# Performance work log

Measured on AMD Instinct MI355X. Metric: run time of the kernel, lower is better.

## Reference

```python
import jax, jax.numpy as jnp
import numpy as np

N_QUBITS = 12
N_LAYERS = 6
BATCH = 512
DIM = 2 ** N_QUBITS


def _apply_1q(psi, G, wire):
    """Apply a single-qubit gate on `wire` (wire 0 = most significant).
    psi: [B, 2^n] complex. G: [2,2] (shared) or [B,2,2] (batched)."""
    B = psi.shape[0]
    left = 2 ** wire
    psi = psi.reshape(B, left, 2, -1)
    if G.ndim == 2:
        psi = jnp.einsum('ij,bxjy->bxiy', G, psi)
    else:
        psi = jnp.einsum('bij,bxjy->bxiy', G, psi)
    return psi.reshape(B, -1)


def _apply_cnot(psi, c, t):
    """CNOT with control c, target t on [B, 2^n] state."""
    B = psi.shape[0]
    ps = psi.reshape((B,) + (2,) * N_QUBITS)
    ca, ta = c + 1, t + 1
    c0 = jnp.take(ps, 0, axis=ca)
    c1 = jnp.take(ps, 1, axis=ca)
    flip_ax = ta if ta < ca else ta - 1
    c1 = jnp.flip(c1, axis=flip_ax)  # X on target within control=1 block
    ps = jnp.stack([c0, c1], axis=ca)
    return ps.reshape(B, -1)


def _circuit(x, weights):
    B = x.shape[0]
    psi = jnp.zeros((B, DIM), jnp.complex64).at[:, 0].set(1.0)

    # AngleEmbedding: RY(x_w) on each wire (batched gate matrices)
    h = 0.5 * x
    c, s = jnp.cos(h).astype(jnp.complex64), jnp.sin(h).astype(jnp.complex64)
    for w in range(N_QUBITS):
        G = jnp.stack([jnp.stack([c[:, w], -s[:, w]], -1),
                       jnp.stack([s[:, w], c[:, w]], -1)], -2)  # [B,2,2]
        psi = _apply_1q(psi, G, w)

    # StronglyEntanglingLayers: Rot(phi,theta,omega) per wire, then ring of CNOTs
    for l in range(N_LAYERS):
        phi, theta, omega = weights[l, :, 0], weights[l, :, 1], weights[l, :, 2]
        ct = jnp.cos(0.5 * theta).astype(jnp.complex64)
        st = jnp.sin(0.5 * theta).astype(jnp.complex64)
        ep = jnp.exp(-0.5j * (phi + omega).astype(jnp.complex64))
        em = jnp.exp(0.5j * (phi - omega).astype(jnp.complex64))
        # Rot = RZ(omega) RY(theta) RZ(phi)
        m00 = ep * ct
        m01 = -em * st
        m10 = jnp.conj(em) * st
        m11 = jnp.conj(ep) * ct
        for w in range(N_QUBITS):
            G = jnp.array([[m00[w], m01[w]], [m10[w], m11[w]]], jnp.complex64)
            psi = _apply_1q(psi, G, w)
        r = l % (N_QUBITS - 1) + 1
        for w in range(N_QUBITS):
            psi = _apply_cnot(psi, w, (w + r) % N_QUBITS)

    # <Z_w> for every wire
    probs = psi.real ** 2 + psi.imag ** 2  # [B, 2^n]
    exps = []
    for w in range(N_QUBITS):
        p = probs.reshape(B, 2 ** w, 2, -1)
        exps.append(p[:, :, 0, :].sum((1, 2)) - p[:, :, 1, :].sum((1, 2)))
    return jnp.stack(exps, -1)  # [B, n_qubits]


def setup_inputs() -> dict:
    key = jax.random.key(0)
    k1, k2, k3, k4 = jax.random.split(key, 4)
    x = jax.random.uniform(k1, (BATCH, N_QUBITS), jnp.float32, -np.pi, np.pi)
    weights = jax.random.uniform(k2, (N_LAYERS, N_QUBITS, 3), jnp.float32, 0.0, 2.0 * np.pi)
    W = jax.random.normal(k3, (1, N_QUBITS), jnp.float32) * 0.3
    b = jax.random.normal(k4, (1,), jnp.float32) * 0.01
    return {"x": x, "weights": weights, "W": W, "b": b}


def reference(x, weights, W, b):
    z = _circuit(x, weights)              # [B, n_qubits]
    y = z @ W.T + b                       # [B, 1]
    return y.squeeze(-1)                  # [B]
```

## Files before the change

### kernel.cpp

```cpp
#include <hip/hip_runtime.h>
#include <stdint.h>

#define NQ 12
#define DIM 4096
#define NLAYERS 6
#define TPB 256

typedef float v2f __attribute__((ext_vector_type(2)));

struct Pass_t {
    uint32_t WT[8];
    uint32_t WL[8];
    uint32_t RT[8];
    uint32_t RL[16];
};
struct Pass10_t {
    uint32_t WT[6];
    uint32_t WL[8];
    uint32_t RT[6];
    uint32_t RL[16];
};
struct CK_t {
    Pass10_t PA;
    Pass_t PB;
    Pass_t P1[NLAYERS];
    uint32_t frow[NQ];
};

constexpr uint32_t G2f(uint32_t k){ return ((k&15u)<<8) | (k&0xF0u) | ((k>>8)&15u); }
constexpr uint32_t G3f(uint32_t k){ return ((k&15u)<<4) | ((k>>4)&15u) | (k&0xF00u); }

constexpr uint32_t ech_reduce(const uint32_t* v, int n, uint32_t x){
    bool ch = true;
    while (ch) {
        ch = false;
        for (int i = 0; i < n; i++)
            if (v[i] && (x ^ v[i]) < x) { x ^= v[i]; ch = true; }
    }
    return x;
}

constexpr Pass_t build_pass(const uint32_t* Mc) {
    Pass_t P{};
    uint32_t rows[12]{};
    rows[0] = 8u;
    int nr = 1;
    uint32_t full[12]{}; int nf = 0; full[nf++] = 8u;
    uint32_t We[4]{};  int nw = 0;
    uint32_t Re[5]{};  int nre = 0;
    {
        uint32_t p0 = 0;
        for (int j = 0; j < 5; j++)
            p0 |= (uint32_t)(__builtin_popcount(8u & Mc[4 + j]) & 1) << j;
        uint32_t r = ech_reduce(Re, nre, p0);
        if (r) Re[nre++] = r;
    }
    for (int slot = 0; slot < 4; slot++) {
        uint32_t chosen = 0;
        for (int relax = 0; relax < 3 && !chosen; relax++) {
            for (uint32_t m = 1; m < 4096u && !chosen; m++) {
                if (m & 8u) continue;
                uint32_t wp = (m >> 4) & 15u;
                uint32_t wr = ech_reduce(We, nw, wp);
                if (relax < 2 && !wr) continue;
                uint32_t rp = 0;
                for (int j = 0; j < 5; j++)
                    rp |= (uint32_t)(__builtin_popcount(m & Mc[4 + j]) & 1) << j;
                uint32_t rr = ech_reduce(Re, nre, rp);
                if (relax < 1 && !rr) continue;
                uint32_t fr = ech_reduce(full, nf, m);
                if (!fr) continue;
                chosen = m; full[nf++] = fr;
                if (wr && nw < 4) We[nw++] = wr;
                if (rr && nre < 5) Re[nre++] = rr;
            }
        }
        rows[nr++] = chosen;
    }
    for (int slot = nr; slot < 12; slot++) {
        for (uint32_t m = 1; m < 4096u; m++) {
            if (m & 8u) continue;
            uint32_t fr = ech_reduce(full, nf, m);
            if (fr) { rows[slot] = m; full[nf++] = fr; break; }
        }
    }
    uint32_t col[12]{}, lmc[12]{};
    for (int j = 0; j < 12; j++) {
        uint32_t c = 0;
        for (int i = 0; i < 12; i++) c |= (uint32_t)((rows[i] >> j) & 1u) << i;
        col[j] = c;
    }
    for (int j = 0; j < 12; j++) {
        uint32_t a = 0, mc = Mc[j];
        for (int q = 0; q < 12; q++) if ((mc >> q) & 1u) a ^= col[q];
        lmc[j] = a;
    }
    for (int j = 0; j < 8; j++) { P.WT[j] = col[4 + j]; P.RT[j] = lmc[4 + j]; }
    for (int j = 0; j < 8; j++) {
        uint32_t a = 0;
        for (int q = 0; q < 3; q++) if ((j >> q) & 1) a ^= col[q];
        P.WL[j] = a;
    }
    for (int l = 0; l < 16; l++) {
        uint32_t a = 0;
        for (int q = 0; q < 4; q++) if ((l >> q) & 1) a ^= lmc[q];
        P.RL[l] = a;
    }
    return P;
}

constexpr Pass10_t build_pass10(const uint32_t* Mc) {
    Pass10_t P{};
    uint32_t rows[10]{};
    rows[0] = 8u;
    int nr = 1;
    uint32_t full[10]{}; int nf = 0; full[nf++] = 8u;
    uint32_t We[4]{};  int nw = 0;
    uint32_t Re[5]{};  int nre = 0;
    {
        uint32_t p0 = 0;
        for (int j = 0; j < 5; j++)
            p0 |= (uint32_t)(__builtin_popcount(8u & Mc[4 + j]) & 1) << j;
        uint32_t r = ech_reduce(Re, nre, p0);
        if (r) Re[nre++] = r;
    }
    for (int slot = 0; slot < 4; slot++) {
        uint32_t chosen = 0;
        for (int relax = 0; relax < 3 && !chosen; relax++) {
            for (uint32_t m = 1; m < 1024u && !chosen; m++) {
                if (m & 8u) continue;
                uint32_t wp = (m >> 4) & 15u;
                uint32_t wr = ech_reduce(We, nw, wp);
                if (relax < 2 && !wr) continue;
                uint32_t rp = 0;
                for (int j = 0; j < 5; j++)
                    rp |= (uint32_t)(__builtin_popcount(m & Mc[4 + j]) & 1) << j;
                uint32_t rr = ech_reduce(Re, nre, rp);
                if (relax < 1 && !rr) continue;
                uint32_t fr = ech_reduce(full, nf, m);
                if (!fr) continue;
                chosen = m; full[nf++] = fr;
                if (wr && nw < 4) We[nw++] = wr;
                if (rr && nre < 5) Re[nre++] = rr;
            }
        }
        rows[nr++] = chosen;
    }
    for (int slot = nr; slot < 10; slot++) {
        for (uint32_t m = 1; m < 1024u; m++) {
            if (m & 8u) continue;
            uint32_t fr = ech_reduce(full, nf, m);
            if (fr) { rows[slot] = m; full[nf++] = fr; break; }
        }
    }
    uint32_t col[10]{}, lmc[10]{};
    for (int j = 0; j < 10; j++) {
        uint32_t c = 0;
        for (int i = 0; i < 10; i++) c |= (uint32_t)((rows[i] >> j) & 1u) << i;
        col[j] = c;
    }
    for (int j = 0; j < 10; j++) {
        uint32_t a = 0, mc = Mc[j];
        for (int q = 0; q < 10; q++) if ((mc >> q) & 1u) a ^= col[q];
        lmc[j] = a;
    }
    for (int j = 0; j < 6; j++) { P.WT[j] = col[4 + j]; P.RT[j] = lmc[4 + j]; }
    for (int j = 0; j < 8; j++) {
        uint32_t a = 0;
        for (int q = 0; q < 3; q++) if ((j >> q) & 1) a ^= col[q];
        P.WL[j] = a;
    }
    for (int l = 0; l < 16; l++) {
        uint32_t a = 0;
        for (int q = 0; q < 4; q++) if ((l >> q) & 1) a ^= lmc[q];
        P.RL[l] = a;
    }
    return P;
}

constexpr CK_t build_ck() {
    CK_t ck{};
    uint32_t Acols[NLAYERS][NQ]{}, Aicol5[NQ]{};
    for (int l = 0; l < NLAYERS; l++) {
        int r = l % (NQ - 1) + 1;
        for (int q = 0; q < NQ; q++) {
            uint32_t v = 1u << q;
            for (int w = NQ - 1; w >= 0; w--) {
                int pc = NQ - 1 - w, pt = NQ - 1 - ((w + r) % NQ);
                v ^= ((v >> pc) & 1u) << pt;
            }
            Acols[l][q] = v;
            if (l == NLAYERS - 1) {
                uint32_t u = 1u << q;
                for (int w = 0; w < NQ; w++) {
                    int pc = NQ - 1 - w, pt = NQ - 1 - ((w + r) % NQ);
                    u ^= ((u >> pc) & 1u) << pt;
                }
                Aicol5[q] = u;
            }
        }
    }
    uint32_t Mc10[10]{};
    for (int j = 0; j < 10; j++) Mc10[j] = G3f(1u << j);
    ck.PA = build_pass10(Mc10);
    uint32_t Mc[12]{};
    for (int j = 0; j < 12; j++) Mc[j] = G2f(1u << j);
    ck.PB = build_pass(Mc);
    for (int l = 1; l < NLAYERS; l++) {
        for (int j = 0; j < 12; j++) Mc[j] = G2f(G3f(Acols[l - 1][j]));
        ck.P1[l] = build_pass(Mc);
    }
    uint32_t Mcol[NQ]{};
    for (int j = 0; j < NQ; j++) {
        uint32_t pj = G3f(G2f(1u << j));
        uint32_t M = 0;
        for (int m = 0; m < NQ; m++) if ((pj >> m) & 1u) M ^= Aicol5[m];
        Mcol[j] = M;
    }
    for (int p = 0; p < NQ; p++) {
        uint32_t s = 0;
        for (int j = 0; j < NQ; j++) s |= ((Mcol[j] >> p) & 1u) << j;
        ck.frow[p] = s;
    }
    return ck;
}
constexpr CK_t CK = build_ck();

template<int Q>
__device__ __forceinline__ void gate_q(v2f (&PRE)[8], v2f (&PIM)[8], float4 m) {
    v2f bx = {m.x, m.x}, by = {m.y, m.y}, bz = {m.z, m.z}, bw = {m.w, m.w};
    #pragma unroll
    for (int j = 0; j < 8; j++) {
        if (j & (1 << Q)) continue;
        int j2 = j | (1 << Q);
        v2f re0 = PRE[j], im0 = PIM[j], re1 = PRE[j2], im1 = PIM[j2];
        PRE[j]  = __builtin_elementwise_fma(bx, re0,
                  __builtin_elementwise_fma(by, -im0,
                  __builtin_elementwise_fma(bz, re1, -bw * im1)));
        PIM[j]  = __builtin_elementwise_fma(bx, im0,
                  __builtin_elementwise_fma(by, re0,
                  __builtin_elementwise_fma(bz, im1, bw * re1)));
        PRE[j2] = __builtin_elementwise_fma(bx, re1,
                  __builtin_elementwise_fma(by, im1,
                  __builtin_elementwise_fma(bz, -re0, -bw * im0)));
        PIM[j2] = __builtin_elementwise_fma(bx, im1,
                  __builtin_elementwise_fma(by, -re1,
                  __builtin_elementwise_fma(bz, -im0, bw * re0)));
    }
}

__device__ __forceinline__ void pack_gate(v2f (&PRE)[8], v2f (&PIM)[8], float4 m) {
    v2f d1 = {-m.y, m.y}, d2 = {m.z, -m.z};
    #pragma unroll
    for (int j = 0; j < 8; j++) {
        v2f RE = PRE[j], IM = PIM[j];
        v2f sR = {RE.y, RE.x}, sI = {IM.y, IM.x};
        PRE[j] = m.x * RE + d1 * IM + d2 * sR - m.w * sI;
        PIM[j] = m.x * IM - d1 * RE + d2 * sI + m.w * sR;
    }
}

__device__ __forceinline__ void pa_pass(v2f (&PRE)[8], v2f (&PIM)[8],
                                        float* buf, uint32_t wb, uint32_t rb) {
    constexpr Pass10_t P = CK.PA;
    v2f* bre = (v2f*)buf;
    v2f* bim = (v2f*)(buf + DIM);
    #pragma unroll
    for (int j = 0; j < 8; j++) {
        uint32_t s = (wb ^ P.WL[j]) >> 1;
        bre[s] = PRE[j]; bim[s] = PIM[j];
    }
    __asm__ volatile("s_waitcnt lgkmcnt(0)" ::: "memory");
    #pragma unroll
    for (int j = 0; j < 8; j++) {
        uint32_t s0 = rb ^ P.RL[j], s1 = rb ^ P.RL[j | 8];
        v2f re, im;
        re.x = buf[s0];       re.y = buf[s1];
        im.x = buf[DIM + s0]; im.y = buf[DIM + s1];
        PRE[j] = re; PIM[j] = im;
    }
}

__device__ __forceinline__ void pb_pass(v2f (&PRE)[8], v2f (&PIM)[8],
                                        float* buf, uint32_t wb, uint32_t rb) {
    constexpr Pass_t P = CK.PB;
    v2f* bre = (v2f*)buf;
    v2f* bim = (v2f*)(buf + DIM);
    __syncthreads();
    #pragma unroll
    for (int j = 0; j < 8; j++) {
        uint32_t s = (wb ^ P.WL[j]) >> 1;
        bre[s] = PRE[j]; bim[s] = PIM[j];
    }
    __syncthreads();
    #pragma unroll
    for (int j = 0; j < 8; j++) {
        uint32_t s0 = rb ^ P.RL[j], s1 = rb ^ P.RL[j | 8];
        v2f re, im;
        re.x = buf[s0];       re.y = buf[s1];
        im.x = buf[DIM + s0]; im.y = buf[DIM + s1];
        PRE[j] = re; PIM[j] = im;
    }
}

__device__ __forceinline__ void rebase_pass(v2f (&PRE)[8], v2f (&PIM)[8],
                                            float* buf, int tid, int l) {
    const Pass_t& P = CK.P1[l];
    uint32_t wb = 0, rb = 0;
    #pragma unroll
    for (int j = 0; j < 8; j++) {
        uint32_t sel = (uint32_t)(-(int)((tid >> j) & 1));
        wb ^= sel & P.WT[j];
        rb ^= sel & P.RT[j];
    }
    v2f* bre = (v2f*)buf;
    v2f* bim = (v2f*)(buf + DIM);
    #pragma unroll
    for (int j = 0; j < 8; j++) {
        uint32_t s = (wb ^ P.WL[j]) >> 1;
        bre[s] = PRE[j]; bim[s] = PIM[j];
    }
    __syncthreads();
    #pragma unroll
    for (int j = 0; j < 8; j++) {
        uint32_t s0 = rb ^ P.RL[j], s1 = rb ^ P.RL[j | 8];
        v2f re, im;
        re.x = buf[s0];       re.y = buf[s1];
        im.x = buf[DIM + s0]; im.y = buf[DIM + s1];
        PRE[j] = re; PIM[j] = im;
    }
}

__global__ __launch_bounds__(TPB) void qsim_kernel(
    const float* __restrict__ x,
    const float* __restrict__ weights,
    const float* __restrict__ Wp,
    const float* __restrict__ bptr,
    float* __restrict__ out)
{
    __shared__ float  lds[2 * 2 * DIM];
    __shared__ float4 smat[NLAYERS * NQ];
    __shared__ float  scs[NQ], sss[NQ];
    __shared__ float  red[4];

    const int tid = threadIdx.x;
    const int b   = blockIdx.x;

    if (tid < NQ) {
        float s_, c_;
        sincosf(0.5f * x[b * NQ + tid], &s_, &c_);
        scs[tid] = c_; sss[tid] = s_;
    }
    if (tid < NLAYERS * NQ) {
        float phi   = weights[tid * 3 + 0];
        float theta = weights[tid * 3 + 1];
        float omega = weights[tid * 3 + 2];
        float st, ct; sincosf(0.5f * theta, &st, &ct);
        float sp, cp; sincosf(0.5f * (phi + omega), &sp, &cp);
        float sm, cm; sincosf(0.5f * (phi - omega), &sm, &cm);
        smat[tid] = make_float4(cp * ct, -sp * ct, -cm * st, -sm * st);
    }
    __syncthreads();

    float base = 1.0f;
    #pragma unroll
    for (int j = 0; j < 8; j++) {
        int w = 7 - j;
        base *= ((tid >> j) & 1) ? sss[w] : scs[w];
    }
    v2f PRE[8], PIM[8];
    float c8 = scs[8], s8 = sss[8];
    #pragma unroll
    for (int j = 0; j < 8; j++) {
        float a = base;
        #pragma unroll
        for (int p = 0; p < 3; p++) {
            int w = NQ - 1 - p;
            a *= ((j >> p) & 1) ? sss[w] : scs[w];
        }
        PRE[j].x = a * c8;  PRE[j].y = a * s8;
        PIM[j].x = 0.0f;    PIM[j].y = 0.0f;
    }

    uint32_t pawb = 0, parb = 0, pbwb = 0, pbrb = 0;
    #pragma unroll
    for (int j = 0; j < 6; j++) {
        uint32_t sel = (uint32_t)(-(int)((tid >> j) & 1));
        pawb ^= sel & CK.PA.WT[j]; parb ^= sel & CK.PA.RT[j];
    }
    #pragma unroll
    for (int j = 0; j < 8; j++) {
        uint32_t sel = (uint32_t)(-(int)((tid >> j) & 1));
        pbwb ^= sel & CK.PB.WT[j]; pbrb ^= sel & CK.PB.RT[j];
    }
    {
        uint32_t wvb = (uint32_t)(tid & 0xC0) << 4;
        pawb |= wvb; parb |= wvb;
    }

    float* bufA = lds;
    float* bufB = lds + 2 * DIM;

    #pragma clang loop unroll(disable)
    for (int l = 0; l < NLAYERS; l++) {
        if (l > 0) rebase_pass(PRE, PIM, bufB, tid, l);
        const int sb = l * NQ;
        gate_q<0>(PRE, PIM, smat[sb + 11]);
        gate_q<1>(PRE, PIM, smat[sb + 10]);
        gate_q<2>(PRE, PIM, smat[sb + 9]);
        pack_gate(PRE, PIM, smat[sb + 8]);
        pa_pass(PRE, PIM, bufA, pawb, parb);
        gate_q<0>(PRE, PIM, smat[sb + 7]);
        gate_q<1>(PRE, PIM, smat[sb + 6]);
        gate_q<2>(PRE, PIM, smat[sb + 5]);
        pack_gate(PRE, PIM, smat[sb + 4]);
        pb_pass(PRE, PIM, bufA, pbwb, pbrb);
        gate_q<0>(PRE, PIM, smat[sb + 3]);
        gate_q<1>(PRE, PIM, smat[sb + 2]);
        gate_q<2>(PRE, PIM, smat[sb + 1]);
        pack_gate(PRE, PIM, smat[sb + 0]);
    }

    const float bv = bptr[0];
    float wbT[NQ];
    #pragma unroll
    for (int p = 0; p < NQ; p++) {
        uint32_t row = CK.frow[p];
        int tp = __popc(tid & (int)(row >> 4)) & 1;
        float Wv = Wp[NQ - 1 - p];
        wbT[p] = tp ? -Wv : Wv;
    }
    v2f acc2 = {0.0f, 0.0f};
    #pragma unroll
    for (int j = 0; j < 8; j++) {
        float cx = bv, cy = bv;
        #pragma unroll
        for (int p = 0; p < NQ; p++) {
            uint32_t row = CK.frow[p];
            float s = (__popc(j & (int)(row & 7u)) & 1) ? -wbT[p] : wbT[p];
            cx += s;
            cy += (row & 8u) ? -s : s;
        }
        v2f c = {cx, cy};
        acc2 += (PRE[j] * PRE[j] + PIM[j] * PIM[j]) * c;
    }
    float acc = acc2.x + acc2.y;
    #pragma unroll
    for (int off = 32; off > 0; off >>= 1)
        acc += __shfl_down(acc, off, 64);
    if ((tid & 63) == 0) red[tid >> 6] = acc;
    __syncthreads();
    if (tid == 0) out[b] = red[0] + red[1] + red[2] + red[3];
}

extern "C" void kernel_launch(void* const* d_in, const int* in_sizes, int n_in,
                              void* d_out, int out_size, void* d_ws, size_t ws_size,
                              hipStream_t stream) {
    const float* x       = (const float*)d_in[0];
    const float* weights = (const float*)d_in[1];
    const float* W       = (const float*)d_in[2];
    const float* bptr    = (const float*)d_in[3];
    qsim_kernel<<<512, TPB, 0, stream>>>(x, weights, W, bptr, (float*)d_out);
}
```

Measured before the change: 91.34 us.

## Choose basis so paired amplitudes sit two apart for fused LDS reads

Extends the compile-time basis-change construction so that, when solvable, it forces the pair partner of each amplitude to be at a fixed offset of 2 floats in LDS. The read phase can then fetch both halves with addresses s0 and s0+2, which the compiler can merge into a single ds_read2 instead of two independent reads with separate address computations. The constrained greedy search may yield different bank-conflict patterns, and passes where the constraint cannot be met fall back to the old path.

Result: slower. 94.29 us (+3.2%).

```diff
diff --git a/kernel.cpp b/kernel.cpp
--- a/kernel.cpp
+++ b/kernel.cpp
@@ -13,12 +13,14 @@
     uint32_t WL[8];
     uint32_t RT[8];
     uint32_t RL[16];
+    uint32_t paired;
 };
 struct Pass10_t {
     uint32_t WT[6];
     uint32_t WL[8];
     uint32_t RT[6];
     uint32_t RL[16];
+    uint32_t paired;
 };
 struct CK_t {
     Pass10_t PA;
@@ -40,14 +42,43 @@
     return x;
 }
 
+constexpr uint32_t solve_y(const uint32_t* Mc, int n) {
+    uint32_t eq[12]{};
+    for (int q = 0; q < n; q++)
+        eq[q] = Mc[q] | ((q == 3 ? 1u : 0u) << n);
+    int r = 0;
+    for (int c = 0; c < n && r < n; c++) {
+        int p = -1;
+        for (int i = r; i < n; i++) if ((eq[i] >> c) & 1u) { p = i; break; }
+        if (p < 0) continue;
+        uint32_t t = eq[p]; eq[p] = eq[r]; eq[r] = t;
+        for (int i = 0; i < n; i++)
+            if (i != r && ((eq[i] >> c) & 1u)) eq[i] ^= eq[r];
+        r++;
+    }
+    uint32_t y = 0;
+    for (int i = 0; i < n; i++) {
+        uint32_t row = eq[i] & ((1u << n) - 1u);
+        if (row && ((eq[i] >> n) & 1u)) {
+            int c = 0; while (!((row >> c) & 1u)) c++;
+            y |= 1u << c;
+        }
+    }
+    return y;
+}
+
 constexpr Pass_t build_pass(const uint32_t* Mc) {
     Pass_t P{};
+    const uint32_t u = Mc[3];
+    uint32_t paired = ((u >> 3) & 1u) ? 0u : 1u;
+    uint32_t y = paired ? solve_y(Mc, 12) : 0u;
+    if (y == 0u || (y & 8u)) paired = 0u;
     uint32_t rows[12]{};
     rows[0] = 8u;
     int nr = 1;
     uint32_t full[12]{}; int nf = 0; full[nf++] = 8u;
-    uint32_t We[4]{};  int nw = 0;
-    uint32_t Re[5]{};  int nre = 0;
+    uint32_t We[5]{};  int nw = 0;
+    uint32_t Re[6]{};  int nre = 0;
     {
         uint32_t p0 = 0;
         for (int j = 0; j < 5; j++)
@@ -55,11 +86,26 @@
         uint32_t r = ech_reduce(Re, nre, p0);
         if (r) Re[nre++] = r;
     }
-    for (int slot = 0; slot < 4; slot++) {
+    if (paired) {
+        rows[nr++] = y;
+        uint32_t fr = ech_reduce(full, nf, y);
+        full[nf++] = fr;
+        uint32_t wp = (y >> 4) & 15u;
+        uint32_t wr = ech_reduce(We, nw, wp);
+        if (wr && nw < 4) We[nw++] = wr;
+        uint32_t rp = 0;
+        for (int j = 0; j < 5; j++)
+            rp |= (uint32_t)(__builtin_popcount(y & Mc[4 + j]) & 1) << j;
+        uint32_t rr = ech_reduce(Re, nre, rp);
+        if (rr && nre < 5) Re[nre++] = rr;
+    }
+    const int ngreedy = 5 - nr;
+    for (int slot = 0; slot < ngreedy; slot++) {
         uint32_t chosen = 0;
         for (int relax = 0; relax < 3 && !chosen; relax++) {
             for (uint32_t m = 1; m < 4096u && !chosen; m++) {
                 if (m & 8u) continue;
+                if (paired && (__builtin_popcount(m & u) & 1)) continue;
                 uint32_t wp = (m >> 4) & 15u;
                 uint32_t wr = ech_reduce(We, nw, wp);
                 if (relax < 2 && !wr) continue;
@@ -80,6 +126,7 @@
     for (int slot = nr; slot < 12; slot++) {
         for (uint32_t m = 1; m < 4096u; m++) {
             if (m & 8u) continue;
+            if (paired && (__builtin_popcount(m & u) & 1)) continue;
             uint32_t fr = ech_reduce(full, nf, m);
             if (fr) { rows[slot] = m; full[nf++] = fr; break; }
         }
@@ -95,6 +142,7 @@
         for (int q = 0; q < 12; q++) if ((mc >> q) & 1u) a ^= col[q];
         lmc[j] = a;
     }
+    if (paired && lmc[3] != 2u) paired = 0;
     for (int j = 0; j < 8; j++) { P.WT[j] = col[4 + j]; P.RT[j] = lmc[4 + j]; }
     for (int j = 0; j < 8; j++) {
         uint32_t a = 0;
@@ -106,17 +154,22 @@
         for (int q = 0; q < 4; q++) if ((l >> q) & 1) a ^= lmc[q];
         P.RL[l] = a;
     }
+    P.paired = paired;
     return P;
 }
 
 constexpr Pass10_t build_pass10(const uint32_t* Mc) {
     Pass10_t P{};
+    const uint32_t u = Mc[3];
+    uint32_t paired = ((u >> 3) & 1u) ? 0u : 1u;
+    uint32_t y = paired ? solve_y(Mc, 10) : 0u;
+    if (y == 0u || (y & 8u)) paired = 0u;
     uint32_t rows[10]{};
     rows[0] = 8u;
     int nr = 1;
     uint32_t full[10]{}; int nf = 0; full[nf++] = 8u;
-    uint32_t We[4]{};  int nw = 0;
-    uint32_t Re[5]{};  int nre = 0;
+    uint32_t We[5]{};  int nw = 0;
+    uint32_t Re[6]{};  int nre = 0;
     {
         uint32_t p0 = 0;
         for (int j = 0; j < 5; j++)
@@ -124,11 +177,26 @@
         uint32_t r = ech_reduce(Re, nre, p0);
         if (r) Re[nre++] = r;
     }
-    for (int slot = 0; slot < 4; slot++) {
+    if (paired) {
+        rows[nr++] = y;
+        uint32_t fr = ech_reduce(full, nf, y);
+        full[nf++] = fr;
+        uint32_t wp = (y >> 4) & 15u;
+        uint32_t wr = ech_reduce(We, nw, wp);
+        if (wr && nw < 4) We[nw++] = wr;
+        uint32_t rp = 0;
+        for (int j = 0; j < 5; j++)
+            rp |= (uint32_t)(__builtin_popcount(y & Mc[4 + j]) & 1) << j;
+        uint32_t rr = ech_reduce(Re, nre, rp);
+        if (rr && nre < 5) Re[nre++] = rr;
+    }
+    const int ngreedy = 5 - nr;
+    for (int slot = 0; slot < ngreedy; slot++) {
         uint32_t chosen = 0;
         for (int relax = 0; relax < 3 && !chosen; relax++) {
             for (uint32_t m = 1; m < 1024u && !chosen; m++) {
                 if (m & 8u) continue;
+                if (paired && (__builtin_popcount(m & u) & 1)) continue;
                 uint32_t wp = (m >> 4) & 15u;
                 uint32_t wr = ech_reduce(We, nw, wp);
                 if (relax < 2 && !wr) continue;
@@ -149,6 +217,7 @@
     for (int slot = nr; slot < 10; slot++) {
         for (uint32_t m = 1; m < 1024u; m++) {
             if (m & 8u) continue;
+            if (paired && (__builtin_popcount(m & u) & 1)) continue;
             uint32_t fr = ech_reduce(full, nf, m);
             if (fr) { rows[slot] = m; full[nf++] = fr; break; }
         }
@@ -164,6 +233,7 @@
         for (int q = 0; q < 10; q++) if ((mc >> q) & 1u) a ^= col[q];
         lmc[j] = a;
     }
+    if (paired && lmc[3] != 2u) paired = 0;
     for (int j = 0; j < 6; j++) { P.WT[j] = col[4 + j]; P.RT[j] = lmc[4 + j]; }
     for (int j = 0; j < 8; j++) {
         uint32_t a = 0;
@@ -175,6 +245,7 @@
         for (int q = 0; q < 4; q++) if ((l >> q) & 1) a ^= lmc[q];
         P.RL[l] = a;
     }
+    P.paired = paired;
     return P;
 }
 
@@ -271,13 +342,24 @@
         bre[s] = PRE[j]; bim[s] = PIM[j];
     }
     __asm__ volatile("s_waitcnt lgkmcnt(0)" ::: "memory");
-    #pragma unroll
-    for (int j = 0; j < 8; j++) {
-        uint32_t s0 = rb ^ P.RL[j], s1 = rb ^ P.RL[j | 8];
-        v2f re, im;
-        re.x = buf[s0];       re.y = buf[s1];
-        im.x = buf[DIM + s0]; im.y = buf[DIM + s1];
-        PRE[j] = re; PIM[j] = im;
+    if (P.paired) {
+        #pragma unroll
+        for (int j = 0; j < 8; j++) {
+            uint32_t s0 = rb ^ P.RL[j];
+            v2f re, im;
+            re.x = buf[s0];       re.y = buf[s0 + 2];
+            im.x = buf[DIM + s0]; im.y = buf[DIM + s0 + 2];
+            PRE[j] = re; PIM[j] = im;
+        }
+    } else {
+        #pragma unroll
+        for (int j = 0; j < 8; j++) {
+            uint32_t s0 = rb ^ P.RL[j], s1 = rb ^ P.RL[j | 8];
+            v2f re, im;
+            re.x = buf[s0];       re.y = buf[s1];
+            im.x = buf[DIM + s0]; im.y = buf[DIM + s1];
+            PRE[j] = re; PIM[j] = im;
+        }
     }
 }
 
@@ -293,13 +375,24 @@
         bre[s] = PRE[j]; bim[s] = PIM[j];
     }
     __syncthreads();
-    #pragma unroll
-    for (int j = 0; j < 8; j++) {
-        uint32_t s0 = rb ^ P.RL[j], s1 = rb ^ P.RL[j | 8];
-        v2f re, im;
-        re.x = buf[s0];       re.y = buf[s1];
-        im.x = buf[DIM + s0]; im.y = buf[DIM + s1];
-        PRE[j] = re; PIM[j] = im;
+    if (P.paired) {
+        #pragma unroll
+        for (int j = 0; j < 8; j++) {
+            uint32_t s0 = rb ^ P.RL[j];
+            v2f re, im;
+            re.x = buf[s0];       re.y = buf[s0 + 2];
+            im.x = buf[DIM + s0]; im.y = buf[DIM + s0 + 2];
+            PRE[j] = re; PIM[j] = im;
+        }
+    } else {
+        #pragma unroll
+        for (int j = 0; j < 8; j++) {
+            uint32_t s0 = rb ^ P.RL[j], s1 = rb ^ P.RL[j | 8];
+            v2f re, im;
+            re.x = buf[s0];       re.y = buf[s1];
+            im.x = buf[DIM + s0]; im.y = buf[DIM + s1];
+            PRE[j] = re; PIM[j] = im;
+        }
     }
 }
 
@@ -321,13 +414,24 @@
         bre[s] = PRE[j]; bim[s] = PIM[j];
     }
     __syncthreads();
-    #pragma unroll
-    for (int j = 0; j < 8; j++) {
-        uint32_t s0 = rb ^ P.RL[j], s1 = rb ^ P.RL[j | 8];
-        v2f re, im;
-        re.x = buf[s0];       re.y = buf[s1];
-        im.x = buf[DIM + s0]; im.y = buf[DIM + s1];
-        PRE[j] = re; PIM[j] = im;
+    if (P.paired) {
+        #pragma unroll
+        for (int j = 0; j < 8; j++) {
+            uint32_t s0 = rb ^ P.RL[j];
+            v2f re, im;
+            re.x = buf[s0];       re.y = buf[s0 + 2];
+            im.x = buf[DIM + s0]; im.y = buf[DIM + s0 + 2];
+            PRE[j] = re; PIM[j] = im;
+        }
+    } else {
+        #pragma unroll
+        for (int j = 0; j < 8; j++) {
+            uint32_t s0 = rb ^ P.RL[j], s1 = rb ^ P.RL[j | 8];
+            v2f re, im;
+            re.x = buf[s0];       re.y = buf[s1];
+            im.x = buf[DIM + s0]; im.y = buf[DIM + s1];
+            PRE[j] = re; PIM[j] = im;
+        }
     }
 }
 
```
